# Kernel tuning notes

Hardware: AMD Instinct MI355X
Metric: run time of the kernel (lower is better)

The kernel has to match this reference:

```python
import jax, jax.numpy as jnp
import numpy as np

EMBED = 512
HEADS = 8
HEAD_DIM = EMBED // HEADS


def setup_inputs() -> dict:
    key = jax.random.key(0)
    ks = jax.random.split(key, 7)
    N, Q, K = 8, 2048, 4096
    s = 1.0 / np.sqrt(EMBED)
    return {
        "x": jax.random.normal(ks[0], (N, Q, EMBED), dtype=jnp.float32),
        "y": jax.random.normal(ks[1], (N, K, EMBED), dtype=jnp.float32),
        "Wq": jax.random.normal(ks[2], (EMBED, EMBED), dtype=jnp.float32) * s,
        "Wk": jax.random.normal(ks[3], (EMBED, EMBED), dtype=jnp.float32) * s,
        "Wv": jax.random.normal(ks[4], (EMBED, EMBED), dtype=jnp.float32) * s,
        "Wo": jax.random.normal(ks[5], (EMBED, EMBED), dtype=jnp.float32) * s,
        "bo": jax.random.normal(ks[6], (EMBED,), dtype=jnp.float32) * 0.01,
    }


def reference(x, y, Wq, Wk, Wv, Wo, bo):
    N, Q, _ = x.shape
    K = y.shape[1]
    # torch Linear: out = in @ W.T
    queries = (x @ Wq.T).reshape(N, Q, HEADS, HEAD_DIM)
    keys = (y @ Wk.T).reshape(N, K, HEADS, HEAD_DIM)
    values = (y @ Wv.T).reshape(N, K, HEADS, HEAD_DIM)
    # NOTE: heads are SUMMED in the score einsum (head-collapsed attention)
    energy = jnp.einsum("nqhd,nkhd->nqk", queries, keys)  # [N,Q,K]
    attention = jax.nn.softmax(energy / jnp.sqrt(jnp.float32(EMBED)), axis=2)
    out = jnp.einsum("nqk,nkhd->nqhd", attention, values).reshape(N, Q, EMBED)
    return x + out @ Wo.T + bo
```

## Files before the change

kernel.cpp:

```cpp
#include <hip/hip_runtime.h>
#include <stdint.h>

typedef unsigned short u16;
typedef short bf16x8 __attribute__((ext_vector_type(8)));
typedef float f32x4 __attribute__((ext_vector_type(4)));
typedef u16 u16x8 __attribute__((ext_vector_type(8)));
typedef u16 u16x4v __attribute__((ext_vector_type(4)));

#define EMBED 512
#define NBATCH 8
#define QLEN 2048
#define KLEN 4096

__device__ __forceinline__ u16 f2bf(float f) {
  uint32_t u = __builtin_bit_cast(uint32_t, f);
  u += 0x7fffu + ((u >> 16) & 1u);
  return (u16)(u >> 16);
}
__device__ __forceinline__ float bf2f(u16 b) {
  return __builtin_bit_cast(float, (uint32_t)b << 16);
}

__device__ __forceinline__ void gload_lds16(const void* g, void* lds) {
  __builtin_amdgcn_global_load_lds(
      (__attribute__((address_space(1))) void*)(uintptr_t)g,
      (__attribute__((address_space(3))) void*)(uint32_t)(uintptr_t)lds,
      16, 0, 0);
}

__global__ __launch_bounds__(256) void cvt_all_kernel(
    const float* __restrict__ x, const float* __restrict__ y,
    const float* __restrict__ wq, const float* __restrict__ wk,
    const float* __restrict__ wv, const float* __restrict__ wo,
    u16* __restrict__ dst) {
  const int64_t B0 = 2097152;
  const int64_t B1 = B0 + 4194304;
  const int64_t B2 = B1 + 65536;
  const int64_t B3 = B2 + 65536;
  const int64_t B4 = B3 + 65536;
  int64_t i = (int64_t)blockIdx.x * 256 + threadIdx.x;
  const float* src; int64_t off;
  if (i < B0)      { src = x;  off = 0;  }
  else if (i < B1) { src = y;  off = B0; }
  else if (i < B2) { src = wq; off = B1; }
  else if (i < B3) { src = wk; off = B2; }
  else if (i < B4) { src = wv; off = B3; }
  else             { src = wo; off = B4; }
  float4 f = ((const float4*)src)[i - off];
  u16x4v o = { f2bf(f.x), f2bf(f.y), f2bf(f.z), f2bf(f.w) };
  ((u16x4v*)dst)[i] = o;
}

constexpr int EPI_BF16 = 0;
constexpr int EPI_BF16_SCALE = 1;
constexpr int EPI_BF16_TRANS = 2;
constexpr int EPI_F32_RESID = 3;

template <int MODE>
__global__ __launch_bounds__(256, 2) void gemm_bt(
    const u16* __restrict__ A, const u16* __restrict__ B, void* __restrict__ Cv,
    int M, int N, int K,
    int64_t aBatch, int64_t bBatch, int64_t cBatch,
    float scale, const float* __restrict__ xres, const float* __restrict__ bias,
    u16* __restrict__ Vt) {
  __shared__ __align__(16) u16 As[128 * 64];
  __shared__ __align__(16) u16 Bs[128 * 64];

  const int tid = threadIdx.x;
  const int wave = tid >> 6;
  const int lane = tid & 63;
  const int bz = blockIdx.z;
  const int row0 = blockIdx.x * 128;
  const int col0 = blockIdx.y * 128;
  const u16* Ab = A + (int64_t)bz * aBatch;
  const u16* Bb = B + (int64_t)bz * bBatch;

  const int srow = wave * 32 + (lane >> 3);
  const int scol = (lane & 7) * 8;
  const u16* aSrc = Ab + (int64_t)(row0 + srow) * K + scol;
  const u16* bSrc = Bb + (int64_t)(col0 + srow) * K + scol;

  const int wm = (wave >> 1) * 64;
  const int wn = (wave & 1) * 64;
  const int fr = lane & 15;
  const int fq = lane >> 4;

  f32x4 acc[4][4];
#pragma unroll
  for (int mi = 0; mi < 4; ++mi)
#pragma unroll
    for (int ni = 0; ni < 4; ++ni) acc[mi][ni] = 0.0f;

  const int nkt = K >> 6;
  for (int kt = 0; kt < nkt; ++kt) {
    __syncthreads();
    const u16* aS = aSrc + kt * 64;
    const u16* bS = bSrc + kt * 64;
#pragma unroll
    for (int i = 0; i < 4; ++i) {
      gload_lds16(aS + (int64_t)(i * 8) * K, &As[(wave * 32 + i * 8) * 64]);
      gload_lds16(bS + (int64_t)(i * 8) * K, &Bs[(wave * 32 + i * 8) * 64]);
    }
    __syncthreads();
#pragma unroll
    for (int ks = 0; ks < 2; ++ks) {
      bf16x8 af[4], bfr[4];
#pragma unroll
      for (int mi = 0; mi < 4; ++mi)
        af[mi] = *(const bf16x8*)&As[(wm + mi * 16 + fr) * 64 + ks * 32 + fq * 8];
#pragma unroll
      for (int ni = 0; ni < 4; ++ni)
        bfr[ni] = *(const bf16x8*)&Bs[(wn + ni * 16 + fr) * 64 + ks * 32 + fq * 8];
#pragma unroll
      for (int mi = 0; mi < 4; ++mi)
#pragma unroll
        for (int ni = 0; ni < 4; ++ni)
          acc[mi][ni] = __builtin_amdgcn_mfma_f32_16x16x32_bf16(af[mi], bfr[ni],
                                                                acc[mi][ni], 0, 0, 0);
    }
  }

  if constexpr (MODE == EPI_BF16 || MODE == EPI_BF16_SCALE) {
    u16* C = (u16*)Cv + (int64_t)bz * cBatch;
#pragma unroll
    for (int mi = 0; mi < 4; ++mi) {
      const int rowb = row0 + wm + mi * 16 + fq * 4;
#pragma unroll
      for (int ni = 0; ni < 4; ++ni) {
        const int col = col0 + wn + ni * 16 + fr;
#pragma unroll
        for (int r = 0; r < 4; ++r) {
          float v = acc[mi][ni][r];
          if constexpr (MODE == EPI_BF16_SCALE) v *= scale;
          C[(int64_t)(rowb + r) * N + col] = f2bf(v);
        }
      }
    }
  } else if constexpr (MODE == EPI_BF16_TRANS) {
#pragma unroll
    for (int mi = 0; mi < 4; ++mi) {
      const int rowb = row0 + wm + mi * 16 + fq * 4;
      const int nb = rowb >> 12;
      const int kk = rowb & 4095;
#pragma unroll
      for (int ni = 0; ni < 4; ++ni) {
        const int col = col0 + wn + ni * 16 + fr;
        u16x4v o = { f2bf(acc[mi][ni][0]), f2bf(acc[mi][ni][1]),
                     f2bf(acc[mi][ni][2]), f2bf(acc[mi][ni][3]) };
        *(u16x4v*)&Vt[((int64_t)nb * EMBED + col) * KLEN + kk] = o;
      }
    }
  } else {
    float* C = (float*)Cv;
#pragma unroll
    for (int mi = 0; mi < 4; ++mi) {
      const int rowb = row0 + wm + mi * 16 + fq * 4;
#pragma unroll
      for (int ni = 0; ni < 4; ++ni) {
        const int col = col0 + wn + ni * 16 + fr;
        const float bv = bias[col];
#pragma unroll
        for (int r = 0; r < 4; ++r) {
          const int64_t idx = (int64_t)(rowb + r) * N + col;
          C[idx] = acc[mi][ni][r] + xres[idx] + bv;
        }
      }
    }
  }
}

__global__ __launch_bounds__(256, 1) void attn_kernel(
    const u16* __restrict__ Qm, const u16* __restrict__ Km,
    const u16* __restrict__ Vt, u16* __restrict__ O) {
  __shared__ __align__(16) u16 Ks[2][32 * 512];
  __shared__ __align__(16) u16 Ps[64 * 32];
  __shared__ __align__(16) float Als[64];

  const int tid = threadIdx.x;
  const int w = tid >> 6;
  const int lane = tid & 63;
  const int fr = lane & 15, fq = lane >> 4;
  const int s7 = fr & 7;
  const int nb = blockIdx.x & 7;
  const int qt = blockIdx.x >> 3;

  bf16x8 q[16];
  {
    const u16* Qb = Qm + ((int64_t)nb * QLEN + qt * 64 + w * 16 + fr) * EMBED + fq * 8;
#pragma unroll
    for (int kc = 0; kc < 16; ++kc) q[kc] = *(const bf16x8*)&Qb[kc * 32];
  }

  f32x4 o[32];
#pragma unroll
  for (int i = 0; i < 32; ++i) o[i] = 0.0f;
  f32x4 mrun, lrun;
#pragma unroll
  for (int r = 0; r < 4; ++r) { mrun[r] = -1e30f; lrun[r] = 0.0f; }

  const u16* Kb = Km + (int64_t)nb * KLEN * EMBED;
  const u16* VbW = Vt + (int64_t)nb * (int64_t)EMBED * KLEN + (int64_t)(w * 128) * KLEN;

  {
    const u16* src = Kb + (int64_t)(w * 8) * EMBED;
#pragma unroll
    for (int i = 0; i < 8; ++i)
      gload_lds16(src + (int64_t)i * EMBED + (lane ^ i) * 8, &Ks[0][(w * 8 + i) * 512]);
  }
  __syncthreads();

  const int NT = KLEN / 32;
  for (int t = 0; t < NT; ++t) {
    const int cur = t & 1;
    if (t + 1 < NT) {
      const u16* src = Kb + ((int64_t)(t + 1) * 32 + w * 8) * EMBED;
#pragma unroll
      for (int i = 0; i < 8; ++i)
        gload_lds16(src + (int64_t)i * EMBED + (lane ^ i) * 8,
                    &Ks[cur ^ 1][(w * 8 + i) * 512]);
    }
    bf16x8 vf[8];
#pragma unroll
    for (int ni = 0; ni < 8; ++ni)
      vf[ni] = *(const bf16x8*)&VbW[(int64_t)(ni * 16 + fr) * KLEN + t * 32 + fq * 8];

    const u16* Kc = Ks[cur];
    f32x4 s[2];
    s[0] = 0.0f; s[1] = 0.0f;
#pragma unroll
    for (int kc = 0; kc < 16; ++kc) {
#pragma unroll
      for (int ni = 0; ni < 2; ++ni) {
        bf16x8 b = *(const bf16x8*)&Kc[(ni * 16 + fr) * 512 + (((kc * 4 + fq) ^ s7) * 8)];
        s[ni] = __builtin_amdgcn_mfma_f32_16x16x32_bf16(q[kc], b, s[ni], 0, 0, 0);
      }
    }

    f32x4 mt;
#pragma unroll
    for (int r = 0; r < 4; ++r) mt[r] = fmaxf(s[0][r], s[1][r]);
#pragma unroll
    for (int off = 1; off <= 8; off <<= 1)
#pragma unroll
      for (int r = 0; r < 4; ++r) mt[r] = fmaxf(mt[r], __shfl_xor(mt[r], off));
    int ok = 1;
#pragma unroll
    for (int r = 0; r < 4; ++r) ok &= (mt[r] <= mrun[r] + 8.0f);
    f32x4 alpha;
    if (__all(ok)) {
#pragma unroll
      for (int r = 0; r < 4; ++r) alpha[r] = 1.0f;
    } else {
#pragma unroll
      for (int r = 0; r < 4; ++r) {
        float mn = fmaxf(mrun[r], mt[r]);
        alpha[r] = __expf(mrun[r] - mn);
        lrun[r] *= alpha[r];
        mrun[r] = mn;
      }
    }
    float p[2][4];
    f32x4 rs;
#pragma unroll
    for (int r = 0; r < 4; ++r) rs[r] = 0.0f;
#pragma unroll
    for (int ni = 0; ni < 2; ++ni)
#pragma unroll
      for (int r = 0; r < 4; ++r) {
        p[ni][r] = __expf(s[ni][r] - mrun[r]);
        rs[r] += p[ni][r];
      }
#pragma unroll
    for (int off = 1; off <= 8; off <<= 1)
#pragma unroll
      for (int r = 0; r < 4; ++r) rs[r] += __shfl_xor(rs[r], off);
#pragma unroll
    for (int r = 0; r < 4; ++r) lrun[r] += rs[r];

#pragma unroll
    for (int ni = 0; ni < 2; ++ni)
#pragma unroll
      for (int r = 0; r < 4; ++r)
        Ps[(w * 16 + fq * 4 + r) * 32 + (((ni * 2 + (fr >> 3)) ^ r ^ fq) * 8) + (fr & 7)]
            = f2bf(p[ni][r]);
    if (fr == 0) {
#pragma unroll
      for (int r = 0; r < 4; ++r) Als[w * 16 + fq * 4 + r] = alpha[r];
    }

    asm volatile("s_waitcnt lgkmcnt(0)" ::: "memory");
    __builtin_amdgcn_sched_barrier(0);
    __builtin_amdgcn_s_barrier();
    __builtin_amdgcn_sched_barrier(0);

    f32x4 ra[4];
#pragma unroll
    for (int mi = 0; mi < 4; ++mi) ra[mi] = *(const f32x4*)&Als[mi * 16 + fq * 4];
    int nz = 0;
#pragma unroll
    for (int mi = 0; mi < 4; ++mi)
#pragma unroll
      for (int r = 0; r < 4; ++r) nz |= (ra[mi][r] != 1.0f);
    if (__any(nz)) {
#pragma unroll
      for (int mi = 0; mi < 4; ++mi)
#pragma unroll
        for (int ni = 0; ni < 8; ++ni)
#pragma unroll
          for (int r = 0; r < 4; ++r) o[mi * 8 + ni][r] *= ra[mi][r];
    }

    bf16x8 ap[4];
#pragma unroll
    for (int mi = 0; mi < 4; ++mi)
      ap[mi] = *(const bf16x8*)&Ps[(mi * 16 + fr) * 32 +
                                   ((fq ^ (fr & 3) ^ ((fr >> 2) & 3)) * 8)];
#pragma unroll
    for (int mi = 0; mi < 4; ++mi)
#pragma unroll
      for (int ni = 0; ni < 8; ++ni)
        o[mi * 8 + ni] = __builtin_amdgcn_mfma_f32_16x16x32_bf16(ap[mi], vf[ni],
                                                                 o[mi * 8 + ni], 0, 0, 0);

    __syncthreads();
  }

  if (fr == 0) {
#pragma unroll
    for (int r = 0; r < 4; ++r) Als[w * 16 + fq * 4 + r] = lrun[r];
  }
  __syncthreads();
  f32x4 li[4];
#pragma unroll
  for (int mi = 0; mi < 4; ++mi) {
    f32x4 lv = *(const f32x4*)&Als[mi * 16 + fq * 4];
#pragma unroll
    for (int r = 0; r < 4; ++r) li[mi][r] = 1.0f / lv[r];
  }
  u16* Ob = O + ((int64_t)nb * QLEN + qt * 64) * EMBED + w * 128;
#pragma unroll
  for (int mi = 0; mi < 4; ++mi)
#pragma unroll
    for (int ni = 0; ni < 8; ++ni)
#pragma unroll
      for (int r = 0; r < 4; ++r)
        Ob[(int64_t)(mi * 16 + fq * 4 + r) * EMBED + ni * 16 + fr] =
            f2bf(o[mi * 8 + ni][r] * li[mi][r]);
}

extern "C" void kernel_launch(void* const* d_in, const int* in_sizes, int n_in,
                              void* d_out, int out_size, void* d_ws, size_t ws_size,
                              hipStream_t stream) {
  const float* x  = (const float*)d_in[0];
  const float* y  = (const float*)d_in[1];
  const float* Wq = (const float*)d_in[2];
  const float* Wk = (const float*)d_in[3];
  const float* Wv = (const float*)d_in[4];
  const float* Wo = (const float*)d_in[5];
  const float* bo = (const float*)d_in[6];
  float* out = (float*)d_out;

  const int64_t nx = (int64_t)NBATCH * QLEN * EMBED;
  const int64_t ny = (int64_t)NBATCH * KLEN * EMBED;
  const int64_t nw = (int64_t)EMBED * EMBED;

  u16* w   = (u16*)d_ws;
  u16* xb  = w;
  u16* O   = w; w += nx;
  u16* yb  = w; w += ny;
  u16* Wqb = w; w += nw;
  u16* Wkb = w; w += nw;
  u16* Wvb = w; w += nw;
  u16* Wob = w; w += nw;
  u16* Qm  = w; w += nx;
  u16* Km  = w; w += ny;
  u16* Vt  = w; w += ny;

  cvt_all_kernel<<<25600, 256, 0, stream>>>(x, y, Wq, Wk, Wv, Wo, xb);

  const float scal = 0.04419417382415922f;
  gemm_bt<EPI_BF16_SCALE><<<dim3(128, 4, 1), 256, 0, stream>>>(
      xb, Wqb, Qm, 16384, EMBED, EMBED, 0, 0, 0, scal, nullptr, nullptr, nullptr);
  gemm_bt<EPI_BF16><<<dim3(256, 4, 1), 256, 0, stream>>>(
      yb, Wkb, Km, 32768, EMBED, EMBED, 0, 0, 0, 1.f, nullptr, nullptr, nullptr);
  gemm_bt<EPI_BF16_TRANS><<<dim3(256, 4, 1), 256, 0, stream>>>(
      yb, Wvb, nullptr, 32768, EMBED, EMBED, 0, 0, 0, 1.f, nullptr, nullptr, Vt);

  attn_kernel<<<NBATCH * 32, 256, 0, stream>>>(Qm, Km, Vt, O);

  gemm_bt<EPI_F32_RESID><<<dim3(128, 4, 1), 256, 0, stream>>>(
      O, Wob, out, 16384, EMBED, EMBED, 0, 0, 0, 1.f, x, bo, nullptr);
}
```

Baseline: 458.8 us.

## Split key sequence across two wave groups per attention block with LDS merge

Result: slower. 1.005 ms (+119.2%).

```diff
diff --git a/kernel.cpp b/kernel.cpp
--- a/kernel.cpp
+++ b/kernel.cpp
@@ -169,15 +169,18 @@
   }
 }
 
-__global__ __launch_bounds__(256, 1) void attn_kernel(
+__global__ __launch_bounds__(512, 2) void attn_kernel(
     const u16* __restrict__ Qm, const u16* __restrict__ Km,
     const u16* __restrict__ Vt, u16* __restrict__ O) {
-  __shared__ __align__(16) u16 Ks[2][32 * 512];
-  __shared__ __align__(16) u16 Ps[64 * 32];
-  __shared__ __align__(16) float Als[64];
+  __shared__ __align__(16) u16 Ks[2][2][32 * 512];
+  __shared__ __align__(16) u16 Ps[2][64 * 32];
+  __shared__ __align__(16) float Als[2][64];
+  __shared__ float Mls[2][64], Lls[2][64];
 
   const int tid = threadIdx.x;
   const int w = tid >> 6;
+  const int g = w >> 2;
+  const int wg = w & 3;
   const int lane = tid & 63;
   const int fr = lane & 15, fq = lane >> 4;
   const int s7 = fr & 7;
@@ -186,7 +189,7 @@
 
   bf16x8 q[16];
   {
-    const u16* Qb = Qm + ((int64_t)nb * QLEN + qt * 64 + w * 16 + fr) * EMBED + fq * 8;
+    const u16* Qb = Qm + ((int64_t)nb * QLEN + qt * 64 + wg * 16 + fr) * EMBED + fq * 8;
 #pragma unroll
     for (int kc = 0; kc < 16; ++kc) q[kc] = *(const bf16x8*)&Qb[kc * 32];
   }
@@ -199,32 +202,36 @@
   for (int r = 0; r < 4; ++r) { mrun[r] = -1e30f; lrun[r] = 0.0f; }
 
   const u16* Kb = Km + (int64_t)nb * KLEN * EMBED;
-  const u16* VbW = Vt + (int64_t)nb * (int64_t)EMBED * KLEN + (int64_t)(w * 128) * KLEN;
+  const u16* VbW = Vt + (int64_t)nb * (int64_t)EMBED * KLEN + (int64_t)(wg * 128) * KLEN;
+
+  const int NT = KLEN / 32 / 2;
+  const int t0 = g * NT;
 
   {
-    const u16* src = Kb + (int64_t)(w * 8) * EMBED;
+    const u16* src = Kb + ((int64_t)t0 * 32 + wg * 8) * EMBED;
 #pragma unroll
     for (int i = 0; i < 8; ++i)
-      gload_lds16(src + (int64_t)i * EMBED + (lane ^ i) * 8, &Ks[0][(w * 8 + i) * 512]);
+      gload_lds16(src + (int64_t)i * EMBED + (lane ^ i) * 8,
+                  &Ks[g][0][(wg * 8 + i) * 512]);
   }
   __syncthreads();
 
-  const int NT = KLEN / 32;
   for (int t = 0; t < NT; ++t) {
     const int cur = t & 1;
+    const int tt = t0 + t;
     if (t + 1 < NT) {
-      const u16* src = Kb + ((int64_t)(t + 1) * 32 + w * 8) * EMBED;
+      const u16* src = Kb + ((int64_t)(tt + 1) * 32 + wg * 8) * EMBED;
 #pragma unroll
       for (int i = 0; i < 8; ++i)
         gload_lds16(src + (int64_t)i * EMBED + (lane ^ i) * 8,
-                    &Ks[cur ^ 1][(w * 8 + i) * 512]);
+                    &Ks[g][cur ^ 1][(wg * 8 + i) * 512]);
     }
     bf16x8 vf[8];
 #pragma unroll
     for (int ni = 0; ni < 8; ++ni)
-      vf[ni] = *(const bf16x8*)&VbW[(int64_t)(ni * 16 + fr) * KLEN + t * 32 + fq * 8];
-
-    const u16* Kc = Ks[cur];
+      vf[ni] = *(const bf16x8*)&VbW[(int64_t)(ni * 16 + fr) * KLEN + tt * 32 + fq * 8];
+
+    const u16* Kc = Ks[g][cur];
     f32x4 s[2];
     s[0] = 0.0f; s[1] = 0.0f;
 #pragma unroll
@@ -281,11 +288,11 @@
     for (int ni = 0; ni < 2; ++ni)
 #pragma unroll
       for (int r = 0; r < 4; ++r)
-        Ps[(w * 16 + fq * 4 + r) * 32 + (((ni * 2 + (fr >> 3)) ^ r ^ fq) * 8) + (fr & 7)]
+        Ps[g][(wg * 16 + fq * 4 + r) * 32 + (((ni * 2 + (fr >> 3)) ^ r ^ fq) * 8) + (fr & 7)]
             = f2bf(p[ni][r]);
     if (fr == 0) {
 #pragma unroll
-      for (int r = 0; r < 4; ++r) Als[w * 16 + fq * 4 + r] = alpha[r];
+      for (int r = 0; r < 4; ++r) Als[g][wg * 16 + fq * 4 + r] = alpha[r];
     }
 
     asm volatile("s_waitcnt lgkmcnt(0)" ::: "memory");
@@ -295,7 +302,7 @@
 
     f32x4 ra[4];
 #pragma unroll
-    for (int mi = 0; mi < 4; ++mi) ra[mi] = *(const f32x4*)&Als[mi * 16 + fq * 4];
+    for (int mi = 0; mi < 4; ++mi) ra[mi] = *(const f32x4*)&Als[g][mi * 16 + fq * 4];
     int nz = 0;
 #pragma unroll
     for (int mi = 0; mi < 4; ++mi)
@@ -313,8 +320,8 @@
     bf16x8 ap[4];
 #pragma unroll
     for (int mi = 0; mi < 4; ++mi)
-      ap[mi] = *(const bf16x8*)&Ps[(mi * 16 + fr) * 32 +
-                                   ((fq ^ (fr & 3) ^ ((fr >> 2) & 3)) * 8)];
+      ap[mi] = *(const bf16x8*)&Ps[g][(mi * 16 + fr) * 32 +
+                                      ((fq ^ (fr & 3) ^ ((fr >> 2) & 3)) * 8)];
 #pragma unroll
     for (int mi = 0; mi < 4; ++mi)
 #pragma unroll
@@ -327,25 +334,56 @@
 
   if (fr == 0) {
 #pragma unroll
-    for (int r = 0; r < 4; ++r) Als[w * 16 + fq * 4 + r] = lrun[r];
+    for (int r = 0; r < 4; ++r) {
+      Mls[g][wg * 16 + fq * 4 + r] = mrun[r];
+      Lls[g][wg * 16 + fq * 4 + r] = lrun[r];
+    }
   }
   __syncthreads();
-  f32x4 li[4];
+
+  f32x4 fac[4];
 #pragma unroll
   for (int mi = 0; mi < 4; ++mi) {
-    f32x4 lv = *(const f32x4*)&Als[mi * 16 + fq * 4];
-#pragma unroll
-    for (int r = 0; r < 4; ++r) li[mi][r] = 1.0f / lv[r];
-  }
-  u16* Ob = O + ((int64_t)nb * QLEN + qt * 64) * EMBED + w * 128;
-#pragma unroll
-  for (int mi = 0; mi < 4; ++mi)
-#pragma unroll
-    for (int ni = 0; ni < 8; ++ni)
-#pragma unroll
-      for (int r = 0; r < 4; ++r)
-        Ob[(int64_t)(mi * 16 + fq * 4 + r) * EMBED + ni * 16 + fr] =
-            f2bf(o[mi * 8 + ni][r] * li[mi][r]);
+#pragma unroll
+    for (int r = 0; r < 4; ++r) {
+      const int row = mi * 16 + fq * 4 + r;
+      const float m0 = Mls[0][row], m1 = Mls[1][row];
+      const float M = fmaxf(m0, m1);
+      const float e0 = __expf(m0 - M), e1 = __expf(m1 - M);
+      const float L = Lls[0][row] * e0 + Lls[1][row] * e1;
+      const float inv = 1.0f / L;
+      fac[mi][r] = (g == 0 ? e0 : e1) * inv;
+    }
+  }
+
+  float* Mb = (float*)&Ks[0][0][0];
+  if (g == 0) {
+#pragma unroll
+    for (int mi = 0; mi < 4; ++mi)
+#pragma unroll
+      for (int ni = 0; ni < 8; ++ni)
+#pragma unroll
+        for (int r = 0; r < 4; ++r)
+          Mb[(mi * 16 + fq * 4 + r) * 512 + wg * 128 + ni * 16 + fr] =
+              o[mi * 8 + ni][r] * fac[mi][r];
+  }
+  __syncthreads();
+
+  if (g == 1) {
+    u16* Ob = O + ((int64_t)nb * QLEN + qt * 64) * EMBED + wg * 128;
+#pragma unroll
+    for (int mi = 0; mi < 4; ++mi)
+#pragma unroll
+      for (int ni = 0; ni < 8; ++ni)
+#pragma unroll
+        for (int r = 0; r < 4; ++r) {
+          const int row = mi * 16 + fq * 4 + r;
+          const int col = ni * 16 + fr;
+          const float v = Mb[row * 512 + wg * 128 + col] +
+                          o[mi * 8 + ni][r] * fac[mi][r];
+          Ob[(int64_t)row * EMBED + col] = f2bf(v);
+        }
+  }
 }
 
 extern "C" void kernel_launch(void* const* d_in, const int* in_sizes, int n_in,
@@ -386,7 +424,7 @@
   gemm_bt<EPI_BF16_TRANS><<<dim3(256, 4, 1), 256, 0, stream>>>(
       yb, Wvb, nullptr, 32768, EMBED, EMBED, 0, 0, 0, 1.f, nullptr, nullptr, Vt);
 
-  attn_kernel<<<NBATCH * 32, 256, 0, stream>>>(Qm, Km, Vt, O);
+  attn_kernel<<<NBATCH * 32, 512, 0, stream>>>(Qm, Km, Vt, O);
 
   gemm_bt<EPI_F32_RESID><<<dim3(128, 4, 1), 256, 0, stream>>>(
       O, Wob, out, 16384, EMBED, EMBED, 0, 0, 0, 1.f, x, bo, nullptr);
```

## Split attention over the key dimension into two chunks and merge partials

Applied to the files above, without the earlier changes.

Result: slower. 484.7 us (+5.7%).

```diff
diff --git a/kernel.cpp b/kernel.cpp
--- a/kernel.cpp
+++ b/kernel.cpp
@@ -171,7 +171,8 @@
 
 __global__ __launch_bounds__(256, 1) void attn_kernel(
     const u16* __restrict__ Qm, const u16* __restrict__ Km,
-    const u16* __restrict__ Vt, u16* __restrict__ O) {
+    const u16* __restrict__ Vt, u16* __restrict__ P1,
+    float* __restrict__ P0, float* __restrict__ Ms, float* __restrict__ Ls) {
   __shared__ __align__(16) u16 Ks[2][32 * 512];
   __shared__ __align__(16) u16 Ps[64 * 32];
   __shared__ __align__(16) float Als[64];
@@ -183,6 +184,7 @@
   const int s7 = fr & 7;
   const int nb = blockIdx.x & 7;
   const int qt = blockIdx.x >> 3;
+  const int g = blockIdx.y;
 
   bf16x8 q[16];
   {
@@ -201,19 +203,22 @@
   const u16* Kb = Km + (int64_t)nb * KLEN * EMBED;
   const u16* VbW = Vt + (int64_t)nb * (int64_t)EMBED * KLEN + (int64_t)(w * 128) * KLEN;
 
+  const int NT = 64;
+  const int t0 = g * NT;
+
   {
-    const u16* src = Kb + (int64_t)(w * 8) * EMBED;
+    const u16* src = Kb + ((int64_t)t0 * 32 + w * 8) * EMBED;
 #pragma unroll
     for (int i = 0; i < 8; ++i)
       gload_lds16(src + (int64_t)i * EMBED + (lane ^ i) * 8, &Ks[0][(w * 8 + i) * 512]);
   }
   __syncthreads();
 
-  const int NT = KLEN / 32;
   for (int t = 0; t < NT; ++t) {
     const int cur = t & 1;
+    const int tt = t0 + t;
     if (t + 1 < NT) {
-      const u16* src = Kb + ((int64_t)(t + 1) * 32 + w * 8) * EMBED;
+      const u16* src = Kb + ((int64_t)(tt + 1) * 32 + w * 8) * EMBED;
 #pragma unroll
       for (int i = 0; i < 8; ++i)
         gload_lds16(src + (int64_t)i * EMBED + (lane ^ i) * 8,
@@ -222,7 +227,7 @@
     bf16x8 vf[8];
 #pragma unroll
     for (int ni = 0; ni < 8; ++ni)
-      vf[ni] = *(const bf16x8*)&VbW[(int64_t)(ni * 16 + fr) * KLEN + t * 32 + fq * 8];
+      vf[ni] = *(const bf16x8*)&VbW[(int64_t)(ni * 16 + fr) * KLEN + tt * 32 + fq * 8];
 
     const u16* Kc = Ks[cur];
     f32x4 s[2];
@@ -327,25 +332,54 @@
 
   if (fr == 0) {
 #pragma unroll
-    for (int r = 0; r < 4; ++r) Als[w * 16 + fq * 4 + r] = lrun[r];
-  }
-  __syncthreads();
-  f32x4 li[4];
-#pragma unroll
-  for (int mi = 0; mi < 4; ++mi) {
-    f32x4 lv = *(const f32x4*)&Als[mi * 16 + fq * 4];
-#pragma unroll
-    for (int r = 0; r < 4; ++r) li[mi][r] = 1.0f / lv[r];
-  }
-  u16* Ob = O + ((int64_t)nb * QLEN + qt * 64) * EMBED + w * 128;
-#pragma unroll
-  for (int mi = 0; mi < 4; ++mi)
-#pragma unroll
-    for (int ni = 0; ni < 8; ++ni)
-#pragma unroll
-      for (int r = 0; r < 4; ++r)
-        Ob[(int64_t)(mi * 16 + fq * 4 + r) * EMBED + ni * 16 + fr] =
-            f2bf(o[mi * 8 + ni][r] * li[mi][r]);
+    for (int r = 0; r < 4; ++r) {
+      const int rowG = nb * QLEN + qt * 64 + w * 16 + fq * 4 + r;
+      Ms[g * 16384 + rowG] = mrun[r];
+      Ls[g * 16384 + rowG] = lrun[r];
+    }
+  }
+  const int64_t base = ((int64_t)nb * QLEN + qt * 64) * EMBED + w * 128;
+  if (g == 0) {
+#pragma unroll
+    for (int mi = 0; mi < 4; ++mi)
+#pragma unroll
+      for (int ni = 0; ni < 8; ++ni)
+#pragma unroll
+        for (int r = 0; r < 4; ++r)
+          P0[base + (int64_t)(mi * 16 + fq * 4 + r) * EMBED + ni * 16 + fr] =
+              o[mi * 8 + ni][r];
+  } else {
+#pragma unroll
+    for (int mi = 0; mi < 4; ++mi)
+#pragma unroll
+      for (int ni = 0; ni < 8; ++ni)
+#pragma unroll
+        for (int r = 0; r < 4; ++r)
+          P1[base + (int64_t)(mi * 16 + fq * 4 + r) * EMBED + ni * 16 + fr] =
+              f2bf(o[mi * 8 + ni][r]);
+  }
+}
+
+__global__ __launch_bounds__(256) void merge_kernel(
+    const float* __restrict__ P0, u16* __restrict__ P1O,
+    const float* __restrict__ Ms, const float* __restrict__ Ls) {
+  const int idx = blockIdx.x * 256 + threadIdx.x;
+  const int row = idx >> 6;
+  const int c = (idx & 63) * 8;
+  const float m0 = Ms[row], m1 = Ms[16384 + row];
+  const float M = fmaxf(m0, m1);
+  float w0 = __expf(m0 - M), w1 = __expf(m1 - M);
+  const float inv = 1.0f / (Ls[row] * w0 + Ls[16384 + row] * w1);
+  w0 *= inv; w1 *= inv;
+  const int64_t off = (int64_t)row * EMBED + c;
+  float4 a0 = *(const float4*)&P0[off];
+  float4 a1 = *(const float4*)&P0[off + 4];
+  u16x8 b = *(const u16x8*)&P1O[off];
+  float av[8] = {a0.x, a0.y, a0.z, a0.w, a1.x, a1.y, a1.z, a1.w};
+  u16x8 ov;
+#pragma unroll
+  for (int j = 0; j < 8; ++j) ov[j] = f2bf(av[j] * w0 + bf2f(b[j]) * w1);
+  *(u16x8*)&P1O[off] = ov;
 }
 
 extern "C" void kernel_launch(void* const* d_in, const int* in_sizes, int n_in,
@@ -376,6 +410,10 @@
   u16* Km  = w; w += ny;
   u16* Vt  = w; w += ny;
 
+  float* P0f = (float*)yb;
+  float* Mst = (float*)Wqb;
+  float* Lst = Mst + 2 * 16384;
+
   cvt_all_kernel<<<25600, 256, 0, stream>>>(x, y, Wq, Wk, Wv, Wo, xb);
 
   const float scal = 0.04419417382415922f;
@@ -386,7 +424,9 @@
   gemm_bt<EPI_BF16_TRANS><<<dim3(256, 4, 1), 256, 0, stream>>>(
       yb, Wvb, nullptr, 32768, EMBED, EMBED, 0, 0, 0, 1.f, nullptr, nullptr, Vt);
 
-  attn_kernel<<<NBATCH * 32, 256, 0, stream>>>(Qm, Km, Vt, O);
+  attn_kernel<<<dim3(256, 2), 256, 0, stream>>>(Qm, Km, Vt, O, P0f, Mst, Lst);
+
+  merge_kernel<<<4096, 256, 0, stream>>>(P0f, O, Mst, Lst);
 
   gemm_bt<EPI_F32_RESID><<<dim3(128, 4, 1), 256, 0, stream>>>(
       O, Wob, out, 16384, EMBED, EMBED, 0, 0, 0, 1.f, x, bo, nullptr);
```

## Keep P in registers via transposed S MFMA and stage V through LDS

Applied to the files above, without the earlier changes.

After: 415.5 us. -9.4%, faster.

```diff
diff --git a/kernel.cpp b/kernel.cpp
--- a/kernel.cpp
+++ b/kernel.cpp
@@ -6,6 +6,7 @@
 typedef float f32x4 __attribute__((ext_vector_type(4)));
 typedef u16 u16x8 __attribute__((ext_vector_type(8)));
 typedef u16 u16x4v __attribute__((ext_vector_type(4)));
+typedef uint32_t u32x4 __attribute__((ext_vector_type(4)));
 
 #define EMBED 512
 #define NBATCH 8
@@ -173,8 +174,7 @@
     const u16* __restrict__ Qm, const u16* __restrict__ Km,
     const u16* __restrict__ Vt, u16* __restrict__ O) {
   __shared__ __align__(16) u16 Ks[2][32 * 512];
-  __shared__ __align__(16) u16 Ps[64 * 32];
-  __shared__ __align__(16) float Als[64];
+  __shared__ __align__(16) u16 Vs[2][512 * 32];
 
   const int tid = threadIdx.x;
   const int w = tid >> 6;
@@ -194,18 +194,24 @@
   f32x4 o[32];
 #pragma unroll
   for (int i = 0; i < 32; ++i) o[i] = 0.0f;
-  f32x4 mrun, lrun;
-#pragma unroll
-  for (int r = 0; r < 4; ++r) { mrun[r] = -1e30f; lrun[r] = 0.0f; }
+  float mrun = -1e30f, lrun = 0.0f;
 
   const u16* Kb = Km + (int64_t)nb * KLEN * EMBED;
-  const u16* VbW = Vt + (int64_t)nb * (int64_t)EMBED * KLEN + (int64_t)(w * 128) * KLEN;
+  const u16* Vb = Vt + (int64_t)nb * (int64_t)EMBED * KLEN;
+
+  const int vrow = lane >> 2;
+  const int vcl = (lane & 3) ^ (vrow & 3);
 
   {
-    const u16* src = Kb + (int64_t)(w * 8) * EMBED;
+    const u16* srcK = Kb + (int64_t)(w * 8) * EMBED;
 #pragma unroll
     for (int i = 0; i < 8; ++i)
-      gload_lds16(src + (int64_t)i * EMBED + (lane ^ i) * 8, &Ks[0][(w * 8 + i) * 512]);
+      gload_lds16(srcK + (int64_t)i * EMBED + (lane ^ i) * 8, &Ks[0][(w * 8 + i) * 512]);
+#pragma unroll
+    for (int i = 0; i < 8; ++i) {
+      const int row0 = w * 128 + i * 16;
+      gload_lds16(Vb + (int64_t)(row0 + vrow) * KLEN + vcl * 8, &Vs[0][row0 * 32]);
+    }
   }
   __syncthreads();
 
@@ -213,139 +219,99 @@
   for (int t = 0; t < NT; ++t) {
     const int cur = t & 1;
     if (t + 1 < NT) {
-      const u16* src = Kb + ((int64_t)(t + 1) * 32 + w * 8) * EMBED;
+      const u16* srcK = Kb + ((int64_t)(t + 1) * 32 + w * 8) * EMBED;
 #pragma unroll
       for (int i = 0; i < 8; ++i)
-        gload_lds16(src + (int64_t)i * EMBED + (lane ^ i) * 8,
+        gload_lds16(srcK + (int64_t)i * EMBED + (lane ^ i) * 8,
                     &Ks[cur ^ 1][(w * 8 + i) * 512]);
-    }
-    bf16x8 vf[8];
-#pragma unroll
-    for (int ni = 0; ni < 8; ++ni)
-      vf[ni] = *(const bf16x8*)&VbW[(int64_t)(ni * 16 + fr) * KLEN + t * 32 + fq * 8];
+#pragma unroll
+      for (int i = 0; i < 8; ++i) {
+        const int row0 = w * 128 + i * 16;
+        gload_lds16(Vb + (int64_t)(row0 + vrow) * KLEN + (t + 1) * 32 + vcl * 8,
+                    &Vs[cur ^ 1][row0 * 32]);
+      }
+    }
 
     const u16* Kc = Ks[cur];
-    f32x4 s[2];
-    s[0] = 0.0f; s[1] = 0.0f;
+    f32x4 s0 = 0.0f, s1 = 0.0f;
 #pragma unroll
     for (int kc = 0; kc < 16; ++kc) {
-#pragma unroll
-      for (int ni = 0; ni < 2; ++ni) {
-        bf16x8 b = *(const bf16x8*)&Kc[(ni * 16 + fr) * 512 + (((kc * 4 + fq) ^ s7) * 8)];
-        s[ni] = __builtin_amdgcn_mfma_f32_16x16x32_bf16(q[kc], b, s[ni], 0, 0, 0);
-      }
-    }
-
-    f32x4 mt;
-#pragma unroll
-    for (int r = 0; r < 4; ++r) mt[r] = fmaxf(s[0][r], s[1][r]);
-#pragma unroll
-    for (int off = 1; off <= 8; off <<= 1)
-#pragma unroll
-      for (int r = 0; r < 4; ++r) mt[r] = fmaxf(mt[r], __shfl_xor(mt[r], off));
-    int ok = 1;
-#pragma unroll
-    for (int r = 0; r < 4; ++r) ok &= (mt[r] <= mrun[r] + 8.0f);
-    f32x4 alpha;
-    if (__all(ok)) {
-#pragma unroll
-      for (int r = 0; r < 4; ++r) alpha[r] = 1.0f;
-    } else {
-#pragma unroll
-      for (int r = 0; r < 4; ++r) {
-        float mn = fmaxf(mrun[r], mt[r]);
-        alpha[r] = __expf(mrun[r] - mn);
-        lrun[r] *= alpha[r];
-        mrun[r] = mn;
-      }
-    }
-    float p[2][4];
-    f32x4 rs;
-#pragma unroll
-    for (int r = 0; r < 4; ++r) rs[r] = 0.0f;
-#pragma unroll
-    for (int ni = 0; ni < 2; ++ni)
-#pragma unroll
-      for (int r = 0; r < 4; ++r) {
-        p[ni][r] = __expf(s[ni][r] - mrun[r]);
-        rs[r] += p[ni][r];
-      }
-#pragma unroll
-    for (int off = 1; off <= 8; off <<= 1)
-#pragma unroll
-      for (int r = 0; r < 4; ++r) rs[r] += __shfl_xor(rs[r], off);
-#pragma unroll
-    for (int r = 0; r < 4; ++r) lrun[r] += rs[r];
-
-#pragma unroll
-    for (int ni = 0; ni < 2; ++ni)
-#pragma unroll
-      for (int r = 0; r < 4; ++r)
-        Ps[(w * 16 + fq * 4 + r) * 32 + (((ni * 2 + (fr >> 3)) ^ r ^ fq) * 8) + (fr & 7)]
-            = f2bf(p[ni][r]);
-    if (fr == 0) {
-#pragma unroll
-      for (int r = 0; r < 4; ++r) Als[w * 16 + fq * 4 + r] = alpha[r];
-    }
-
-    asm volatile("s_waitcnt lgkmcnt(0)" ::: "memory");
-    __builtin_amdgcn_sched_barrier(0);
-    __builtin_amdgcn_s_barrier();
-    __builtin_amdgcn_sched_barrier(0);
-
-    f32x4 ra[4];
-#pragma unroll
-    for (int mi = 0; mi < 4; ++mi) ra[mi] = *(const f32x4*)&Als[mi * 16 + fq * 4];
-    int nz = 0;
-#pragma unroll
-    for (int mi = 0; mi < 4; ++mi)
-#pragma unroll
-      for (int r = 0; r < 4; ++r) nz |= (ra[mi][r] != 1.0f);
-    if (__any(nz)) {
-#pragma unroll
-      for (int mi = 0; mi < 4; ++mi)
-#pragma unroll
-        for (int ni = 0; ni < 8; ++ni)
-#pragma unroll
-          for (int r = 0; r < 4; ++r) o[mi * 8 + ni][r] *= ra[mi][r];
-    }
-
-    bf16x8 ap[4];
-#pragma unroll
-    for (int mi = 0; mi < 4; ++mi)
-      ap[mi] = *(const bf16x8*)&Ps[(mi * 16 + fr) * 32 +
-                                   ((fq ^ (fr & 3) ^ ((fr >> 2) & 3)) * 8)];
-#pragma unroll
-    for (int mi = 0; mi < 4; ++mi)
-#pragma unroll
-      for (int ni = 0; ni < 8; ++ni)
-        o[mi * 8 + ni] = __builtin_amdgcn_mfma_f32_16x16x32_bf16(ap[mi], vf[ni],
-                                                                 o[mi * 8 + ni], 0, 0, 0);
+      bf16x8 k0 = *(const bf16x8*)&Kc[(fr)*512 + (((kc * 4 + fq) ^ s7) * 8)];
+      bf16x8 k1 = *(const bf16x8*)&Kc[(16 + fr) * 512 + (((kc * 4 + fq) ^ s7) * 8)];
+      s0 = __builtin_amdgcn_mfma_f32_16x16x32_bf16(k0, q[kc], s0, 0, 0, 0);
+      s1 = __builtin_amdgcn_mfma_f32_16x16x32_bf16(k1, q[kc], s1, 0, 0, 0);
+    }
+
+    float mt = fmaxf(fmaxf(fmaxf(s0[0], s0[1]), fmaxf(s0[2], s0[3])),
+                     fmaxf(fmaxf(s1[0], s1[1]), fmaxf(s1[2], s1[3])));
+    mt = fmaxf(mt, __shfl_xor(mt, 16));
+    mt = fmaxf(mt, __shfl_xor(mt, 32));
+    float alpha = 1.0f;
+    if (!__all(mt <= mrun + 8.0f)) {
+      const float mn = fmaxf(mrun, mt);
+      alpha = __expf(mrun - mn);
+      lrun *= alpha;
+      mrun = mn;
+    }
+    float p0[4], p1[4];
+    float rs = 0.0f;
+#pragma unroll
+    for (int r = 0; r < 4; ++r) {
+      p0[r] = __expf(s0[r] - mrun);
+      p1[r] = __expf(s1[r] - mrun);
+      rs += p0[r] + p1[r];
+    }
+    rs += __shfl_xor(rs, 16);
+    rs += __shfl_xor(rs, 32);
+    lrun += rs;
+
+    const uint32_t lo0 = (uint32_t)f2bf(p0[0]) | ((uint32_t)f2bf(p0[1]) << 16);
+    const uint32_t lo1 = (uint32_t)f2bf(p0[2]) | ((uint32_t)f2bf(p0[3]) << 16);
+    const uint32_t hi0 = (uint32_t)f2bf(p1[0]) | ((uint32_t)f2bf(p1[1]) << 16);
+    const uint32_t hi1 = (uint32_t)f2bf(p1[2]) | ((uint32_t)f2bf(p1[3]) << 16);
+    const int srcA = fr + (((fq << 1) & 3) << 4);
+    const int srcB = srcA + 16;
+    const bool useHi = (fq >= 2);
+    const uint32_t aLo0 = __shfl(lo0, srcA), aHi0 = __shfl(hi0, srcA);
+    const uint32_t aLo1 = __shfl(lo1, srcA), aHi1 = __shfl(hi1, srcA);
+    const uint32_t bLo0 = __shfl(lo0, srcB), bHi0 = __shfl(hi0, srcB);
+    const uint32_t bLo1 = __shfl(lo1, srcB), bHi1 = __shfl(hi1, srcB);
+    u32x4 pd;
+    pd[0] = useHi ? aHi0 : aLo0;
+    pd[1] = useHi ? aHi1 : aLo1;
+    pd[2] = useHi ? bHi0 : bLo0;
+    pd[3] = useHi ? bHi1 : bLo1;
+    const bf16x8 pb = __builtin_bit_cast(bf16x8, pd);
+
+    if (__any(alpha != 1.0f)) {
+      float ra[4];
+#pragma unroll
+      for (int r = 0; r < 4; ++r) ra[r] = __shfl(alpha, (fq << 2) + r);
+#pragma unroll
+      for (int dt = 0; dt < 32; ++dt)
+#pragma unroll
+        for (int r = 0; r < 4; ++r) o[dt][r] *= ra[r];
+    }
+
+    const u16* Vc = Vs[cur];
+#pragma unroll
+    for (int dt = 0; dt < 32; ++dt) {
+      bf16x8 vb = *(const bf16x8*)&Vc[(dt * 16 + fr) * 32 + ((fq ^ (fr & 3)) * 8)];
+      o[dt] = __builtin_amdgcn_mfma_f32_16x16x32_bf16(pb, vb, o[dt], 0, 0, 0);
+    }
 
     __syncthreads();
   }
 
-  if (fr == 0) {
-#pragma unroll
-    for (int r = 0; r < 4; ++r) Als[w * 16 + fq * 4 + r] = lrun[r];
-  }
-  __syncthreads();
-  f32x4 li[4];
-#pragma unroll
-  for (int mi = 0; mi < 4; ++mi) {
-    f32x4 lv = *(const f32x4*)&Als[mi * 16 + fq * 4];
-#pragma unroll
-    for (int r = 0; r < 4; ++r) li[mi][r] = 1.0f / lv[r];
-  }
-  u16* Ob = O + ((int64_t)nb * QLEN + qt * 64) * EMBED + w * 128;
-#pragma unroll
-  for (int mi = 0; mi < 4; ++mi)
-#pragma unroll
-    for (int ni = 0; ni < 8; ++ni)
-#pragma unroll
-      for (int r = 0; r < 4; ++r)
-        Ob[(int64_t)(mi * 16 + fq * 4 + r) * EMBED + ni * 16 + fr] =
-            f2bf(o[mi * 8 + ni][r] * li[mi][r]);
+  float linv[4];
+#pragma unroll
+  for (int r = 0; r < 4; ++r) linv[r] = 1.0f / __shfl(lrun, (fq << 2) + r);
+  u16* Ob = O + ((int64_t)nb * QLEN + qt * 64 + w * 16) * EMBED;
+#pragma unroll
+  for (int dt = 0; dt < 32; ++dt)
+#pragma unroll
+    for (int r = 0; r < 4; ++r)
+      Ob[(int64_t)((fq << 2) + r) * EMBED + dt * 16 + fr] = f2bf(o[dt][r] * linv[r]);
 }
 
 extern "C" void kernel_launch(void* const* d_in, const int* in_sizes, int n_in,
```
